# Kernel tuning notes

Measured on AMD Instinct MI355X. Metric: run time of the kernel, lower is better.

## Reference

```python
import jax, jax.numpy as jnp
import numpy as np

B, S, H = 2, 2048, 1024
NH, HD = 16, 64
EPS = 1e-12
SCALE = float(np.sqrt(HD))


def layer_norm(x, g, b, eps=EPS):
    m = jnp.mean(x, axis=-1, keepdims=True)
    v = jnp.mean(jnp.square(x - m), axis=-1, keepdims=True)
    return (x - m) * jax.lax.rsqrt(v + eps) * g + b


def setup_inputs() -> dict:
    key = jax.random.key(0)
    ks = jax.random.split(key, 12)
    std = 0.02 / np.sqrt(2 * 24)  # num_hidden_layers = 24
    return {
        "hidden_states": jax.random.normal(ks[0], (B, S, H), dtype=jnp.float32),
        "attention_mask": jnp.ones((B, S), dtype=jnp.float32),
        "Wq": jax.random.normal(ks[1], (H, H), dtype=jnp.float32) * std,
        "bq": jnp.zeros((H,), dtype=jnp.float32),
        "Wk": jax.random.normal(ks[2], (H, H), dtype=jnp.float32) * std,
        "bk": jnp.zeros((H,), dtype=jnp.float32),
        "Wv": jax.random.normal(ks[3], (H, H), dtype=jnp.float32) * std,
        "bv": jnp.zeros((H,), dtype=jnp.float32),
        "Wd": jax.random.normal(ks[4], (H, H), dtype=jnp.float32) * (1.0 / np.sqrt(H)),
        "bd": jnp.zeros((H,), dtype=jnp.float32),
        "ln_g": jnp.ones((H,), dtype=jnp.float32),
        "ln_b": jnp.zeros((H,), dtype=jnp.float32),
    }


def reference(hidden_states, attention_mask, Wq, bq, Wk, bk, Wv, bv, Wd, bd, ln_g, ln_b):
    x = hidden_states
    # NOTE: source computes pre_attention_norm(x) but the no-cache path uses raw x for Q/K/V.
    def heads(t):  # [B,S,H] -> [B,NH,S,HD]
        return t.reshape(B, S, NH, HD).transpose(0, 2, 1, 3)

    q = heads(x @ Wq.T + bq)
    k = heads(x @ Wk.T + bk)
    v = heads(x @ Wv.T + bv)

    scores = jnp.einsum("bhqd,bhkd->bhqk", q, k) / SCALE
    mask = (1.0 - attention_mask) * -10000.0  # [B,S] -> broadcast [B,1,1,S]
    scores = scores + mask[:, None, None, :]
    probs = jax.nn.softmax(scores.astype(jnp.float32), axis=-1).astype(x.dtype)

    ctx = jnp.einsum("bhqk,bhkd->bhqd", probs, v)
    ctx = ctx.transpose(0, 2, 1, 3).reshape(B, S, NH * HD)

    out = ctx @ Wd.T + bd
    out = layer_norm(out + x, ln_g, ln_b)
    out = jnp.where(jnp.isfinite(out), out, jnp.zeros_like(out))
    return out
```

## Files before the change

kernel.cpp:

```cpp
#include <hip/hip_runtime.h>
#include <cstdint>
#include <cstddef>

#define B_    2
#define S_    2048
#define H_    1024
#define NH_   16
#define HD_   64

typedef __attribute__((ext_vector_type(8))) __bf16 bf16x8;
typedef __attribute__((ext_vector_type(4))) __bf16 bf16x4;
typedef __attribute__((ext_vector_type(4))) float  f32x4;
typedef __attribute__((ext_vector_type(2))) unsigned u32x2;

typedef __attribute__((address_space(1))) const unsigned int gcu32_t;
typedef __attribute__((address_space(3))) unsigned int lu32_t;
#define GLOAD16(gp, lp) __builtin_amdgcn_global_load_lds((gcu32_t*)(gp), (lu32_t*)(lp), 16, 0, 0)

#if __has_builtin(__builtin_amdgcn_exp2f)
#define EXP2F(x) __builtin_amdgcn_exp2f(x)
#else
#define EXP2F(x) exp2f(x)
#endif

#define SC_Q 0.1803368977f

__device__ __forceinline__ short f2bf(float f) {
  union { float f; unsigned u; } v; v.f = f;
  unsigned r = v.u + 0x7fffu + ((v.u >> 16) & 1u);
  return (short)(r >> 16);
}

__global__ __launch_bounds__(256) void convert_kernel(
    const float* __restrict__ x,  const float* __restrict__ wq,
    const float* __restrict__ wk, const float* __restrict__ wv,
    const float* __restrict__ wd,
    short* __restrict__ xb,  short* __restrict__ wqb, short* __restrict__ wkb,
    short* __restrict__ wvb, short* __restrict__ wdb) {
  size_t i = ((size_t)blockIdx.x * 256 + threadIdx.x) * 4;
  const float* src; short* dst; size_t off;
  if      (i < 4194304u) { src = x;  dst = xb;  off = i; }
  else if (i < 5242880u) { src = wq; dst = wqb; off = i - 4194304u; }
  else if (i < 6291456u) { src = wk; dst = wkb; off = i - 5242880u; }
  else if (i < 7340032u) { src = wv; dst = wvb; off = i - 6291456u; }
  else                   { src = wd; dst = wdb; off = i - 7340032u; }
  float4 v = *(const float4*)(src + off);
  short4 o; o.x = f2bf(v.x); o.y = f2bf(v.y); o.z = f2bf(v.z); o.w = f2bf(v.w);
  *(short4*)(dst + off) = o;
}

template<int MODE>
__global__ __launch_bounds__(256, 3) void gemm_bt(
    const short* __restrict__ A,
    const short* __restrict__ Bq, const short* __restrict__ Bk,
    const short* __restrict__ Bv,
    const float* __restrict__ biasq, const float* __restrict__ biask,
    const float* __restrict__ biasv,
    short* __restrict__ outq, short* __restrict__ outk, short* __restrict__ outv,
    float* __restrict__ outy) {
  __shared__ short As[128 * 64];
  __shared__ short Bs[128 * 64];

  const short* Bw; const float* bias; short* outs = nullptr;
  float qscale = 1.0f;
  if (MODE == 0) {
    int z = blockIdx.z;
    Bw   = (z == 0) ? Bq    : ((z == 1) ? Bk    : Bv);
    bias = (z == 0) ? biasq : ((z == 1) ? biask : biasv);
    outs = (z == 0) ? outq  : ((z == 1) ? outk  : outv);
    if (z == 0) qscale = SC_Q;
  } else {
    Bw = Bq; bias = biasq;
  }

  const int K = 1024;
  int tid  = threadIdx.x;
  int lane = tid & 63, w = tid >> 6;
  int wr = w >> 1, wc = w & 1;
  int m0 = blockIdx.y * 128, n0 = blockIdx.x * 128;
  int l15 = lane & 15, lg = lane >> 4;

  int lr = lane >> 3, lc8 = 8 * ((lane & 7) ^ lr);
  const short* Ag = A  + (size_t)(m0 + w * 8 + lr) * K + lc8;
  const short* Bg = Bw + (size_t)(n0 + w * 8 + lr) * K + lc8;

  int cxor = (l15 & 7) * 8;

  f32x4 acc[4][4];
  for (int m = 0; m < 4; m++)
    for (int n = 0; n < 4; n++) acc[m][n] = {0.f, 0.f, 0.f, 0.f};

  for (int kt = 0; kt < 16; kt++) {
    __syncthreads();
    for (int it = 0; it < 4; it++) {
      GLOAD16(Ag + (size_t)it * 32 * K + kt * 64, &As[(w * 8 + it * 32) * 64]);
      GLOAD16(Bg + (size_t)it * 32 * K + kt * 64, &Bs[(w * 8 + it * 32) * 64]);
    }
    __syncthreads();
#pragma unroll
    for (int kkh = 0; kkh < 2; kkh++) {
      int col = (kkh * 32 + lg * 8) ^ cxor;
      bf16x8 af[4], bfr[4];
#pragma unroll
      for (int m = 0; m < 4; m++)
        af[m] = *(const bf16x8*)&As[(wr * 64 + m * 16 + l15) * 64 + col];
#pragma unroll
      for (int n = 0; n < 4; n++)
        bfr[n] = *(const bf16x8*)&Bs[(wc * 64 + n * 16 + l15) * 64 + col];
#pragma unroll
      for (int m = 0; m < 4; m++)
#pragma unroll
        for (int n = 0; n < 4; n++)
          acc[m][n] = __builtin_amdgcn_mfma_f32_16x16x32_bf16(af[m], bfr[n], acc[m][n], 0, 0, 0);
    }
  }

  for (int n = 0; n < 4; n++) {
    int col = n0 + wc * 64 + n * 16 + l15;
    float bval = bias[col];
    if (MODE == 0) {
      int h = col >> 6, d = col & 63;
      for (int m = 0; m < 4; m++) {
        int rowb = m0 + wr * 64 + m * 16 + lg * 4;
        for (int j = 0; j < 4; j++) {
          int row = rowb + j;
          int bb = row >> 11, s = row & 2047;
          outs[(((size_t)bb * NH_ + h) * S_ + s) * HD_ + d] = f2bf((acc[m][n][j] + bval) * qscale);
        }
      }
    } else {
      for (int m = 0; m < 4; m++) {
        int rowb = m0 + wr * 64 + m * 16 + lg * 4;
        for (int j = 0; j < 4; j++)
          outy[(size_t)(rowb + j) * 1024 + col] = acc[m][n][j] + bval;
      }
    }
  }
}

__global__ __launch_bounds__(512, 4) void attn_kernel(
    const short* __restrict__ Q, const short* __restrict__ K,
    const short* __restrict__ V, const float* __restrict__ mask,
    short* __restrict__ ctx) {
  __shared__ short QPs[128 * 72];
  __shared__ short Ks[2][64 * 64];
  __shared__ short Vs[2][64 * 64];
  __shared__ float msk[2][64];

  int b = blockIdx.x;
  int bh = (b & 7) * 4 + ((b >> 3) >> 4);
  int qb = (b >> 3) & 15;
  int bidx = bh >> 4, h = bh & 15;
  int q0 = qb * 128;
  int tid = threadIdx.x, lane = tid & 63, w = tid >> 6;
  int l15 = lane & 15, lg = lane >> 4;

  const short* Qg = Q + (size_t)bh * S_ * HD_;
  const short* Kg = K + (size_t)bh * S_ * HD_;
  const short* Vg = V + (size_t)bh * S_ * HD_;

  int lr = lane >> 3, lc8 = 8 * ((lane & 7) ^ lr);
  int cxor = (l15 & 7) * 8;
  const float MLOG2E = -10000.0f * 1.442695041f;

#pragma unroll
  for (int it = 0; it < 2; it++) {
    int r = w * 8 + it * 64;
    GLOAD16(Qg + (size_t)(q0 + r + lr) * HD_ + lc8, &QPs[r * 64]);
  }
  GLOAD16(Kg + (size_t)(w * 8 + lr) * HD_ + lc8, &Ks[0][(w * 8) * 64]);
  int vrow = tid >> 3, vcol = (tid & 7) * 8;
  int voff = ((vrow >> 2) * 4 + (vcol >> 4)) * 64 + (vrow & 3) * 16 + (vcol & 15);
  *(int4*)&Vs[0][voff] = *(const int4*)&Vg[(size_t)vrow * HD_ + vcol];
  if (tid < 64) msk[0][tid] = (1.0f - mask[bidx * S_ + tid]) * MLOG2E;
  __syncthreads();

  bf16x8 qreg[2];
#pragma unroll
  for (int kkh = 0; kkh < 2; kkh++) {
    int row = w * 16 + l15;
    qreg[kkh] = *(const bf16x8*)&QPs[row * 64 + ((kkh * 32 + lg * 8) ^ cxor)];
  }
  __syncthreads();

  float mrun = -1e30f, lrun = 0.f;
  f32x4 oacc[4];
#pragma unroll
  for (int dt = 0; dt < 4; dt++) oacc[dt] = {0.f, 0.f, 0.f, 0.f};

  unsigned vtrbase = (unsigned)(uintptr_t)&Vs[0][0] + (unsigned)(lg * 1024 + l15 * 8);
  int psrow = (w * 16 + l15) * 72;

  for (int kt = 0; kt < 32; kt++) {
    int cur = kt & 1;

    int4 vp0; float mp = 0.f;
    if (kt < 31) {
      const short* Kn = Kg + (size_t)(kt + 1) * 64 * HD_;
      GLOAD16(Kn + (size_t)(w * 8 + lr) * HD_ + lc8, &Ks[cur ^ 1][(w * 8) * 64]);
      const short* Vn = Vg + (size_t)(kt + 1) * 64 * HD_;
      vp0 = *(const int4*)&Vn[(size_t)vrow * HD_ + vcol];
      if (tid < 64) mp = (1.0f - mask[bidx * S_ + (kt + 1) * 64 + tid]) * MLOG2E;
    }

    f32x4 sc[4];
#pragma unroll
    for (int n = 0; n < 4; n++) sc[n] = {0.f, 0.f, 0.f, 0.f};
    __builtin_amdgcn_s_setprio(1);
#pragma unroll
    for (int kkh = 0; kkh < 2; kkh++) {
      int col = (kkh * 32 + lg * 8) ^ cxor;
      bf16x8 kbf[4];
#pragma unroll
      for (int n = 0; n < 4; n++)
        kbf[n] = *(const bf16x8*)&Ks[cur][(n * 16 + l15) * 64 + col];
#pragma unroll
      for (int n = 0; n < 4; n++)
        sc[n] = __builtin_amdgcn_mfma_f32_16x16x32_bf16(kbf[n], qreg[kkh], sc[n], 0, 0, 0);
    }
    __builtin_amdgcn_s_setprio(0);

    float pm[4];
#pragma unroll
    for (int n = 0; n < 4; n++) {
      f32x4 mv = *(const f32x4*)&msk[cur][n * 16 + lg * 4];
      float t0 = sc[n][0] + mv[0];
      float t1 = sc[n][1] + mv[1];
      float t2 = sc[n][2] + mv[2];
      float t3 = sc[n][3] + mv[3];
      sc[n][0] = t0; sc[n][1] = t1; sc[n][2] = t2; sc[n][3] = t3;
      pm[n] = fmaxf(fmaxf(t0, t1), fmaxf(t2, t3));
    }
    float rmax = fmaxf(fmaxf(pm[0], pm[1]), fmaxf(pm[2], pm[3]));
    rmax = fmaxf(rmax, __shfl_xor(rmax, 16));
    rmax = fmaxf(rmax, __shfl_xor(rmax, 32));

    if (__any(rmax > mrun + 8.f)) {
      float mn = fmaxf(mrun, rmax);
      float a = EXP2F(mrun - mn);
      lrun *= a;
      mrun = mn;
#pragma unroll
      for (int dt = 0; dt < 4; dt++)
#pragma unroll
        for (int j = 0; j < 4; j++) oacc[dt][j] *= a;
    }

    float rs_ = 0.f;
#pragma unroll
    for (int n = 0; n < 4; n++)
#pragma unroll
      for (int j = 0; j < 4; j++) {
        float p = EXP2F(sc[n][j] - mrun);
        sc[n][j] = p;
        rs_ += p;
      }

#pragma unroll
    for (int n = 0; n < 4; n++) {
      unsigned pk0, pk1;
      asm("v_cvt_pk_bf16_f32 %0, %1, %2" : "=v"(pk0) : "v"(sc[n][0]), "v"(sc[n][1]));
      asm("v_cvt_pk_bf16_f32 %0, %1, %2" : "=v"(pk1) : "v"(sc[n][2]), "v"(sc[n][3]));
      u32x2 wv2; wv2[0] = pk0; wv2[1] = pk1;
      *(u32x2*)&QPs[psrow + n * 16 + lg * 4] = wv2;
    }

    rs_ += __shfl_xor(rs_, 16);
    rs_ += __shfl_xor(rs_, 32);
    lrun += rs_;

    unsigned vtr = vtrbase + (unsigned)(cur * 8192);
#pragma unroll
    for (int kb2 = 0; kb2 < 2; kb2++) {
      bf16x4 vlo[4], vhi[4];
#pragma unroll
      for (int dt = 0; dt < 4; dt++) {
        unsigned a = vtr + (unsigned)(kb2 * 4096 + dt * 128);
        asm volatile("ds_read_b64_tr_b16 %0, %2\n\t"
                     "ds_read_b64_tr_b16 %1, %2 offset:512"
                     : "=v"(vlo[dt]), "=v"(vhi[dt]) : "v"(a));
      }
      bf16x8 pb = *(const bf16x8*)&QPs[psrow + kb2 * 32 + lg * 8];
      asm volatile("s_waitcnt lgkmcnt(0)" ::: "memory");
      __builtin_amdgcn_sched_barrier(0);
      __builtin_amdgcn_s_setprio(1);
#pragma unroll
      for (int dt = 0; dt < 4; dt++) {
        bf16x8 vb = __builtin_shufflevector(vlo[dt], vhi[dt], 0, 1, 2, 3, 4, 5, 6, 7);
        oacc[dt] = __builtin_amdgcn_mfma_f32_16x16x32_bf16(vb, pb, oacc[dt], 0, 0, 0);
      }
      __builtin_amdgcn_s_setprio(0);
    }

    if (kt < 31) {
      *(int4*)&Vs[cur ^ 1][voff] = vp0;
      if (tid < 64) msk[cur ^ 1][tid] = mp;
    }
    __syncthreads();
  }

  float inv = 1.0f / lrun;
  int sg = q0 + w * 16 + l15;
  size_t rowbase = ((size_t)(bidx * S_ + sg)) * H_ + h * HD_;
#pragma unroll
  for (int dt = 0; dt < 4; dt++) {
    short4 st;
    st.x = f2bf(oacc[dt][0] * inv);
    st.y = f2bf(oacc[dt][1] * inv);
    st.z = f2bf(oacc[dt][2] * inv);
    st.w = f2bf(oacc[dt][3] * inv);
    *(short4*)&ctx[rowbase + dt * 16 + lg * 4] = st;
  }
}

__global__ __launch_bounds__(256) void ln_kernel(
    const float* __restrict__ y, const float* __restrict__ x,
    const float* __restrict__ g, const float* __restrict__ bta,
    float* __restrict__ out) {
  __shared__ float red[4];
  int row = blockIdx.x;
  int tid = threadIdx.x, lane = tid & 63, w = tid >> 6;
  size_t base = (size_t)row * 1024 + tid * 4;
  float4 yv = *(const float4*)(y + base);
  float4 xv = *(const float4*)(x + base);
  float v0 = yv.x + xv.x, v1 = yv.y + xv.y, v2 = yv.z + xv.z, v3 = yv.w + xv.w;

  float ssum = v0 + v1 + v2 + v3;
  for (int off = 1; off < 64; off <<= 1) ssum += __shfl_xor(ssum, off);
  if (lane == 0) red[w] = ssum;
  __syncthreads();
  float mean = (red[0] + red[1] + red[2] + red[3]) * (1.f / 1024.f);
  __syncthreads();

  float d0 = v0 - mean, d1 = v1 - mean, d2 = v2 - mean, d3 = v3 - mean;
  float sq = d0 * d0 + d1 * d1 + d2 * d2 + d3 * d3;
  for (int off = 1; off < 64; off <<= 1) sq += __shfl_xor(sq, off);
  if (lane == 0) red[w] = sq;
  __syncthreads();
  float var = (red[0] + red[1] + red[2] + red[3]) * (1.f / 1024.f);
  float rs = 1.0f / sqrtf(var + 1e-12f);

  int c = tid * 4;
  float4 gv = *(const float4*)(g + c);
  float4 bv = *(const float4*)(bta + c);
  float o0 = d0 * rs * gv.x + bv.x;
  float o1 = d1 * rs * gv.y + bv.y;
  float o2 = d2 * rs * gv.z + bv.z;
  float o3 = d3 * rs * gv.w + bv.w;
  float4 ov;
  ov.x = __builtin_isfinite(o0) ? o0 : 0.f;
  ov.y = __builtin_isfinite(o1) ? o1 : 0.f;
  ov.z = __builtin_isfinite(o2) ? o2 : 0.f;
  ov.w = __builtin_isfinite(o3) ? o3 : 0.f;
  *(float4*)(out + base) = ov;
}

extern "C" void kernel_launch(void* const* d_in, const int* in_sizes, int n_in,
                              void* d_out, int out_size, void* d_ws, size_t ws_size,
                              hipStream_t stream) {
  (void)in_sizes; (void)n_in; (void)out_size; (void)ws_size;
  const float* x    = (const float*)d_in[0];
  const float* mask = (const float*)d_in[1];
  const float* Wq   = (const float*)d_in[2];
  const float* bq   = (const float*)d_in[3];
  const float* Wk   = (const float*)d_in[4];
  const float* bk   = (const float*)d_in[5];
  const float* Wv   = (const float*)d_in[6];
  const float* bv   = (const float*)d_in[7];
  const float* Wd   = (const float*)d_in[8];
  const float* bd   = (const float*)d_in[9];
  const float* ln_g = (const float*)d_in[10];
  const float* ln_b = (const float*)d_in[11];
  float* out = (float*)d_out;

  char* ws = (char*)d_ws;
  short* xb   = (short*)(ws);
  short* wqb  = (short*)(ws + ( 8ull << 20));
  short* wkb  = (short*)(ws + (10ull << 20));
  short* wvb  = (short*)(ws + (12ull << 20));
  short* wdb  = (short*)(ws + (14ull << 20));
  short* qb   = (short*)(ws + (16ull << 20));
  short* kb   = (short*)(ws + (24ull << 20));
  short* vb   = (short*)(ws + (32ull << 20));
  short* ctxb = (short*)(ws + (40ull << 20));
  float* y    = (float*)(ws + (48ull << 20));

  convert_kernel<<<8192, 256, 0, stream>>>(x, Wq, Wk, Wv, Wd, xb, wqb, wkb, wvb, wdb);
  gemm_bt<0><<<dim3(8, 32, 3), 256, 0, stream>>>(xb, wqb, wkb, wvb, bq, bk, bv,
                                                 qb, kb, vb, nullptr);
  attn_kernel<<<512, 512, 0, stream>>>(qb, kb, vb, mask, ctxb);
  gemm_bt<1><<<dim3(8, 32, 1), 256, 0, stream>>>(ctxb, wdb, nullptr, nullptr, bd,
                                                 nullptr, nullptr, nullptr, nullptr,
                                                 nullptr, y);
  ln_kernel<<<4096, 256, 0, stream>>>(y, x, ln_g, ln_b, out);
}
```

Baseline: 226.6 us.

## Rewrite attention with 32x32x16 MFMA, register-resident P, and bitmask masking

The attention kernel moves from 16x16x32 to 32x32x16 bf16 MFMAs, with each wave owning 32 query rows and 4 waves per block instead of 8. Probabilities are repacked in registers with v_permlane32_swap instead of a round trip through shared memory, and Q is loaded straight into registers. The additive float mask becomes a precomputed ballot bitmask that is applied only when a tile contains masked keys. This cuts LDS traffic and synchronisation, at the cost of fewer waves per block, more registers per thread, and masked scores forced to -1e30 rather than offset by -10000, which changes results for partially masked rows.

New measurement: 218.8 us. -3.4%, faster.

```diff
diff --git a/kernel.cpp b/kernel.cpp
--- a/kernel.cpp
+++ b/kernel.cpp
@@ -8,10 +8,11 @@
 #define NH_   16
 #define HD_   64
 
-typedef __attribute__((ext_vector_type(8))) __bf16 bf16x8;
-typedef __attribute__((ext_vector_type(4))) __bf16 bf16x4;
-typedef __attribute__((ext_vector_type(4))) float  f32x4;
-typedef __attribute__((ext_vector_type(2))) unsigned u32x2;
+typedef __attribute__((ext_vector_type(8)))  __bf16 bf16x8;
+typedef __attribute__((ext_vector_type(4)))  __bf16 bf16x4;
+typedef __attribute__((ext_vector_type(4)))  float  f32x4;
+typedef __attribute__((ext_vector_type(16))) float  f32x16;
+typedef __attribute__((ext_vector_type(4)))  unsigned u32x4;
 
 typedef __attribute__((address_space(1))) const unsigned int gcu32_t;
 typedef __attribute__((address_space(3))) unsigned int lu32_t;
@@ -138,179 +139,194 @@
   }
 }
 
-__global__ __launch_bounds__(512, 4) void attn_kernel(
+__global__ __launch_bounds__(256, 2) void attn_kernel(
     const short* __restrict__ Q, const short* __restrict__ K,
     const short* __restrict__ V, const float* __restrict__ mask,
     short* __restrict__ ctx) {
-  __shared__ short QPs[128 * 72];
   __shared__ short Ks[2][64 * 64];
   __shared__ short Vs[2][64 * 64];
-  __shared__ float msk[2][64];
+  __shared__ unsigned long long mbits[32];
 
   int b = blockIdx.x;
   int bh = (b & 7) * 4 + ((b >> 3) >> 4);
   int qb = (b >> 3) & 15;
-  int bidx = bh >> 4, h = bh & 15;
+  int bidx = bh >> 4, hh = bh & 15;
   int q0 = qb * 128;
   int tid = threadIdx.x, lane = tid & 63, w = tid >> 6;
-  int l15 = lane & 15, lg = lane >> 4;
+  int l31 = lane & 31, lh = lane >> 5, l15 = lane & 15;
 
   const short* Qg = Q + (size_t)bh * S_ * HD_;
   const short* Kg = K + (size_t)bh * S_ * HD_;
   const short* Vg = V + (size_t)bh * S_ * HD_;
 
   int lr = lane >> 3, lc8 = 8 * ((lane & 7) ^ lr);
-  int cxor = (l15 & 7) * 8;
-  const float MLOG2E = -10000.0f * 1.442695041f;
-
-#pragma unroll
-  for (int it = 0; it < 2; it++) {
-    int r = w * 8 + it * 64;
-    GLOAD16(Qg + (size_t)(q0 + r + lr) * HD_ + lc8, &QPs[r * 64]);
-  }
+  int kxor = (lane & 7) * 8;
+
+  const short* Qrow = Qg + (size_t)(q0 + w * 32 + l31) * HD_;
+  bf16x8 qfrag[4];
+#pragma unroll
+  for (int ks = 0; ks < 4; ks++)
+    qfrag[ks] = *(const bf16x8*)&Qrow[ks * 16 + lh * 8];
+
   GLOAD16(Kg + (size_t)(w * 8 + lr) * HD_ + lc8, &Ks[0][(w * 8) * 64]);
+  GLOAD16(Kg + (size_t)(w * 8 + 32 + lr) * HD_ + lc8, &Ks[0][(w * 8 + 32) * 64]);
   int vrow = tid >> 3, vcol = (tid & 7) * 8;
   int voff = ((vrow >> 2) * 4 + (vcol >> 4)) * 64 + (vrow & 3) * 16 + (vcol & 15);
-  *(int4*)&Vs[0][voff] = *(const int4*)&Vg[(size_t)vrow * HD_ + vcol];
-  if (tid < 64) msk[0][tid] = (1.0f - mask[bidx * S_ + tid]) * MLOG2E;
-  __syncthreads();
-
-  bf16x8 qreg[2];
-#pragma unroll
-  for (int kkh = 0; kkh < 2; kkh++) {
-    int row = w * 16 + l15;
-    qreg[kkh] = *(const bf16x8*)&QPs[row * 64 + ((kkh * 32 + lg * 8) ^ cxor)];
+  *(int4*)&Vs[0][voff]        = *(const int4*)&Vg[(size_t)vrow * HD_ + vcol];
+  *(int4*)&Vs[0][voff + 2048] = *(const int4*)&Vg[(size_t)(vrow + 32) * HD_ + vcol];
+  if (w == 0) {
+#pragma unroll 4
+    for (int t = 0; t < 32; t++) {
+      unsigned long long bb = __ballot(mask[bidx * S_ + t * 64 + lane] > 0.5f);
+      if (lane == 0) mbits[t] = bb;
+    }
   }
   __syncthreads();
 
   float mrun = -1e30f, lrun = 0.f;
-  f32x4 oacc[4];
-#pragma unroll
-  for (int dt = 0; dt < 4; dt++) oacc[dt] = {0.f, 0.f, 0.f, 0.f};
-
-  unsigned vtrbase = (unsigned)(uintptr_t)&Vs[0][0] + (unsigned)(lg * 1024 + l15 * 8);
-  int psrow = (w * 16 + l15) * 72;
+  f32x16 oacc[2];
+#pragma unroll
+  for (int dt = 0; dt < 2; dt++)
+#pragma unroll
+    for (int j = 0; j < 16; j++) oacc[dt][j] = 0.f;
+
+  unsigned vtrb = (unsigned)(uintptr_t)&Vs[0][0]
+                + (unsigned)(l15 * 8 + ((lane >> 4) & 1) * 128 + lh * 1024);
 
   for (int kt = 0; kt < 32; kt++) {
     int cur = kt & 1;
 
-    int4 vp0; float mp = 0.f;
+    int4 vp0, vp1;
     if (kt < 31) {
       const short* Kn = Kg + (size_t)(kt + 1) * 64 * HD_;
       GLOAD16(Kn + (size_t)(w * 8 + lr) * HD_ + lc8, &Ks[cur ^ 1][(w * 8) * 64]);
+      GLOAD16(Kn + (size_t)(w * 8 + 32 + lr) * HD_ + lc8, &Ks[cur ^ 1][(w * 8 + 32) * 64]);
       const short* Vn = Vg + (size_t)(kt + 1) * 64 * HD_;
       vp0 = *(const int4*)&Vn[(size_t)vrow * HD_ + vcol];
-      if (tid < 64) mp = (1.0f - mask[bidx * S_ + (kt + 1) * 64 + tid]) * MLOG2E;
-    }
-
-    f32x4 sc[4];
-#pragma unroll
-    for (int n = 0; n < 4; n++) sc[n] = {0.f, 0.f, 0.f, 0.f};
+      vp1 = *(const int4*)&Vn[(size_t)(vrow + 32) * HD_ + vcol];
+    }
+
+    f32x16 sc[2];
+#pragma unroll
+    for (int kb = 0; kb < 2; kb++)
+#pragma unroll
+      for (int j = 0; j < 16; j++) sc[kb][j] = 0.f;
     __builtin_amdgcn_s_setprio(1);
 #pragma unroll
-    for (int kkh = 0; kkh < 2; kkh++) {
-      int col = (kkh * 32 + lg * 8) ^ cxor;
-      bf16x8 kbf[4];
-#pragma unroll
-      for (int n = 0; n < 4; n++)
-        kbf[n] = *(const bf16x8*)&Ks[cur][(n * 16 + l15) * 64 + col];
-#pragma unroll
-      for (int n = 0; n < 4; n++)
-        sc[n] = __builtin_amdgcn_mfma_f32_16x16x32_bf16(kbf[n], qreg[kkh], sc[n], 0, 0, 0);
-    }
+    for (int ks = 0; ks < 4; ks++)
+#pragma unroll
+      for (int kb = 0; kb < 2; kb++) {
+        bf16x8 af = *(const bf16x8*)&Ks[cur][(kb * 32 + l31) * 64 + ((ks * 16 + lh * 8) ^ kxor)];
+        sc[kb] = __builtin_amdgcn_mfma_f32_32x32x16_bf16(af, qfrag[ks], sc[kb], 0, 0, 0);
+      }
     __builtin_amdgcn_s_setprio(0);
 
-    float pm[4];
-#pragma unroll
-    for (int n = 0; n < 4; n++) {
-      f32x4 mv = *(const f32x4*)&msk[cur][n * 16 + lg * 4];
-      float t0 = sc[n][0] + mv[0];
-      float t1 = sc[n][1] + mv[1];
-      float t2 = sc[n][2] + mv[2];
-      float t3 = sc[n][3] + mv[3];
-      sc[n][0] = t0; sc[n][1] = t1; sc[n][2] = t2; sc[n][3] = t3;
-      pm[n] = fmaxf(fmaxf(t0, t1), fmaxf(t2, t3));
-    }
-    float rmax = fmaxf(fmaxf(pm[0], pm[1]), fmaxf(pm[2], pm[3]));
-    rmax = fmaxf(rmax, __shfl_xor(rmax, 16));
-    rmax = fmaxf(rmax, __shfl_xor(rmax, 32));
+    unsigned long long mb = mbits[kt];
+    if (__any(mb != ~0ull)) {
+      unsigned long long sh = mb >> (lh * 4);
+#pragma unroll
+      for (int kb = 0; kb < 2; kb++)
+#pragma unroll
+        for (int r = 0; r < 16; r++)
+          if (!((sh >> (kb * 32 + (r & 3) + 8 * (r >> 2))) & 1)) sc[kb][r] = -1e30f;
+    }
+
+    float rmax = sc[0][0];
+#pragma unroll
+    for (int kb = 0; kb < 2; kb++)
+#pragma unroll
+      for (int r = 0; r < 16; r++) rmax = fmaxf(rmax, sc[kb][r]);
+    {
+      float xa = rmax, xb = rmax;
+      asm volatile("v_permlane32_swap_b32 %0, %1" : "+v"(xa), "+v"(xb));
+      rmax = fmaxf(xa, xb);
+    }
 
     if (__any(rmax > mrun + 8.f)) {
       float mn = fmaxf(mrun, rmax);
       float a = EXP2F(mrun - mn);
-      lrun *= a;
-      mrun = mn;
-#pragma unroll
-      for (int dt = 0; dt < 4; dt++)
-#pragma unroll
-        for (int j = 0; j < 4; j++) oacc[dt][j] *= a;
+      lrun *= a; mrun = mn;
+#pragma unroll
+      for (int dt = 0; dt < 2; dt++)
+#pragma unroll
+        for (int j = 0; j < 16; j++) oacc[dt][j] *= a;
     }
 
     float rs_ = 0.f;
 #pragma unroll
-    for (int n = 0; n < 4; n++)
-#pragma unroll
-      for (int j = 0; j < 4; j++) {
-        float p = EXP2F(sc[n][j] - mrun);
-        sc[n][j] = p;
+    for (int kb = 0; kb < 2; kb++)
+#pragma unroll
+      for (int r = 0; r < 16; r++) {
+        float p = EXP2F(sc[kb][r] - mrun);
+        sc[kb][r] = p;
         rs_ += p;
       }
-
-#pragma unroll
-    for (int n = 0; n < 4; n++) {
-      unsigned pk0, pk1;
-      asm("v_cvt_pk_bf16_f32 %0, %1, %2" : "=v"(pk0) : "v"(sc[n][0]), "v"(sc[n][1]));
-      asm("v_cvt_pk_bf16_f32 %0, %1, %2" : "=v"(pk1) : "v"(sc[n][2]), "v"(sc[n][3]));
-      u32x2 wv2; wv2[0] = pk0; wv2[1] = pk1;
-      *(u32x2*)&QPs[psrow + n * 16 + lg * 4] = wv2;
-    }
-
-    rs_ += __shfl_xor(rs_, 16);
-    rs_ += __shfl_xor(rs_, 32);
+    {
+      float xa = rs_, xb = rs_;
+      asm volatile("v_permlane32_swap_b32 %0, %1" : "+v"(xa), "+v"(xb));
+      rs_ = xa + xb;
+    }
     lrun += rs_;
 
-    unsigned vtr = vtrbase + (unsigned)(cur * 8192);
-#pragma unroll
-    for (int kb2 = 0; kb2 < 2; kb2++) {
+    bf16x8 pfrag[4];
+#pragma unroll
+    for (int ks = 0; ks < 4; ks++) {
+      int kb = ks >> 1, ro = (ks & 1) * 8;
+      unsigned X0, X1, X2, X3;
+      asm("v_cvt_pk_bf16_f32 %0, %1, %2" : "=v"(X0) : "v"(sc[kb][ro + 0]), "v"(sc[kb][ro + 1]));
+      asm("v_cvt_pk_bf16_f32 %0, %1, %2" : "=v"(X1) : "v"(sc[kb][ro + 2]), "v"(sc[kb][ro + 3]));
+      asm("v_cvt_pk_bf16_f32 %0, %1, %2" : "=v"(X2) : "v"(sc[kb][ro + 4]), "v"(sc[kb][ro + 5]));
+      asm("v_cvt_pk_bf16_f32 %0, %1, %2" : "=v"(X3) : "v"(sc[kb][ro + 6]), "v"(sc[kb][ro + 7]));
+      asm volatile("v_permlane32_swap_b32 %0, %1" : "+v"(X0), "+v"(X2));
+      asm volatile("v_permlane32_swap_b32 %0, %1" : "+v"(X1), "+v"(X3));
+      union { u32x4 u; bf16x8 b; } cvt;
+      cvt.u[0] = X0; cvt.u[1] = X1; cvt.u[2] = X2; cvt.u[3] = X3;
+      pfrag[ks] = cvt.b;
+    }
+
+#pragma unroll
+    for (int dt = 0; dt < 2; dt++) {
       bf16x4 vlo[4], vhi[4];
 #pragma unroll
-      for (int dt = 0; dt < 4; dt++) {
-        unsigned a = vtr + (unsigned)(kb2 * 4096 + dt * 128);
+      for (int ks = 0; ks < 4; ks++) {
+        unsigned a = vtrb + (unsigned)(cur * 8192 + ks * 2048 + dt * 256);
         asm volatile("ds_read_b64_tr_b16 %0, %2\n\t"
                      "ds_read_b64_tr_b16 %1, %2 offset:512"
-                     : "=v"(vlo[dt]), "=v"(vhi[dt]) : "v"(a));
-      }
-      bf16x8 pb = *(const bf16x8*)&QPs[psrow + kb2 * 32 + lg * 8];
+                     : "=&v"(vlo[ks]), "=&v"(vhi[ks]) : "v"(a));
+      }
       asm volatile("s_waitcnt lgkmcnt(0)" ::: "memory");
       __builtin_amdgcn_sched_barrier(0);
       __builtin_amdgcn_s_setprio(1);
 #pragma unroll
-      for (int dt = 0; dt < 4; dt++) {
-        bf16x8 vb = __builtin_shufflevector(vlo[dt], vhi[dt], 0, 1, 2, 3, 4, 5, 6, 7);
-        oacc[dt] = __builtin_amdgcn_mfma_f32_16x16x32_bf16(vb, pb, oacc[dt], 0, 0, 0);
+      for (int ks = 0; ks < 4; ks++) {
+        bf16x8 vb = __builtin_shufflevector(vlo[ks], vhi[ks], 0, 1, 2, 3, 4, 5, 6, 7);
+        oacc[dt] = __builtin_amdgcn_mfma_f32_32x32x16_bf16(vb, pfrag[ks], oacc[dt], 0, 0, 0);
       }
       __builtin_amdgcn_s_setprio(0);
     }
 
     if (kt < 31) {
-      *(int4*)&Vs[cur ^ 1][voff] = vp0;
-      if (tid < 64) msk[cur ^ 1][tid] = mp;
+      *(int4*)&Vs[cur ^ 1][voff]        = vp0;
+      *(int4*)&Vs[cur ^ 1][voff + 2048] = vp1;
     }
     __syncthreads();
   }
 
   float inv = 1.0f / lrun;
-  int sg = q0 + w * 16 + l15;
-  size_t rowbase = ((size_t)(bidx * S_ + sg)) * H_ + h * HD_;
-#pragma unroll
-  for (int dt = 0; dt < 4; dt++) {
-    short4 st;
-    st.x = f2bf(oacc[dt][0] * inv);
-    st.y = f2bf(oacc[dt][1] * inv);
-    st.z = f2bf(oacc[dt][2] * inv);
-    st.w = f2bf(oacc[dt][3] * inv);
-    *(short4*)&ctx[rowbase + dt * 16 + lg * 4] = st;
-  }
+  int q = q0 + w * 32 + l31;
+  size_t base = ((size_t)(bidx * S_ + q)) * H_ + hh * HD_;
+#pragma unroll
+  for (int dt = 0; dt < 2; dt++)
+#pragma unroll
+    for (int rr = 0; rr < 4; rr++) {
+      int d0 = dt * 32 + rr * 8 + lh * 4;
+      short4 st;
+      st.x = f2bf(oacc[dt][rr * 4 + 0] * inv);
+      st.y = f2bf(oacc[dt][rr * 4 + 1] * inv);
+      st.z = f2bf(oacc[dt][rr * 4 + 2] * inv);
+      st.w = f2bf(oacc[dt][rr * 4 + 3] * inv);
+      *(short4*)&ctx[base + d0] = st;
+    }
 }
 
 __global__ __launch_bounds__(256) void ln_kernel(
@@ -388,7 +404,7 @@
   convert_kernel<<<8192, 256, 0, stream>>>(x, Wq, Wk, Wv, Wd, xb, wqb, wkb, wvb, wdb);
   gemm_bt<0><<<dim3(8, 32, 3), 256, 0, stream>>>(xb, wqb, wkb, wvb, bq, bk, bv,
                                                  qb, kb, vb, nullptr);
-  attn_kernel<<<512, 512, 0, stream>>>(qb, kb, vb, mask, ctxb);
+  attn_kernel<<<512, 256, 0, stream>>>(qb, kb, vb, mask, ctxb);
   gemm_bt<1><<<dim3(8, 32, 1), 256, 0, stream>>>(ctxb, wdb, nullptr, nullptr, bd,
                                                  nullptr, nullptr, nullptr, nullptr,
                                                  nullptr, y);
```
